# Optimization experiments

Measured on AMD Instinct MI355X. Metric: run time of the kernel, lower is better.

The kernel has to match this reference:

```python
import jax, jax.numpy as jnp
import numpy as np

N, E, G = 50000, 800000, 64
NODE_DIM, EDGE_DIM, HIDDEN, L = 64, 16, 128, 4


def setup_inputs() -> dict:
    key = jax.random.key(0)
    ks = jax.random.split(key, 24)
    s = 0.05
    inp = {
        "x": jax.random.normal(ks[0], (N, NODE_DIM), jnp.float32),
        "pos": jax.random.normal(ks[1], (N, 3), jnp.float32),
        "edge_attr": jax.random.normal(ks[2], (E, EDGE_DIM), jnp.float32),
        "edge_index": jax.random.randint(ks[3], (2, E), 0, N),
        "batch": jnp.sort(jax.random.randint(ks[4], (N,), 0, G)),
        # node encoder
        "enc_W": jax.random.normal(ks[5], (NODE_DIM, HIDDEN), jnp.float32) * s,
        "enc_b": jnp.zeros((HIDDEN,), jnp.float32),
        # per-layer EGNN params, stacked on leading L axis
        "eW1": jax.random.normal(ks[6], (L, 2 * HIDDEN + EDGE_DIM + 1, HIDDEN), jnp.float32) * s,
        "eb1": jnp.zeros((L, HIDDEN), jnp.float32),
        "eW2": jax.random.normal(ks[7], (L, HIDDEN, HIDDEN), jnp.float32) * s,
        "eb2": jnp.zeros((L, HIDDEN), jnp.float32),
        "nW1": jax.random.normal(ks[8], (L, 2 * HIDDEN, HIDDEN), jnp.float32) * s,
        "nb1": jnp.zeros((L, HIDDEN), jnp.float32),
        "nW2": jax.random.normal(ks[9], (L, HIDDEN, HIDDEN), jnp.float32) * s,
        "nb2": jnp.zeros((L, HIDDEN), jnp.float32),
        # readout MLP (hidden*3 -> hidden -> hidden//2 -> 1)
        "rW1": jax.random.normal(ks[10], (3 * HIDDEN, HIDDEN), jnp.float32) * s,
        "rb1": jnp.zeros((HIDDEN,), jnp.float32),
        "rW2": jax.random.normal(ks[11], (HIDDEN, HIDDEN // 2), jnp.float32) * s,
        "rb2": jnp.zeros((HIDDEN // 2,), jnp.float32),
        "rW3": jax.random.normal(ks[12], (HIDDEN // 2, 1), jnp.float32) * s,
        "rb3": jnp.zeros((1,), jnp.float32),
    }
    return inp


def reference(x, pos, edge_attr, enc_W, enc_b, eW1, eb1, eW2, eb2,
              nW1, nb1, nW2, nb2, rW1, rb1, rW2, rb2, rW3, rb3,
              edge_index, batch):
    relu = jax.nn.relu
    src = edge_index[0]  # j (source) in PyG source_to_target flow
    dst = edge_index[1]  # i (target)

    # node encoder (dropout in eval mode = identity)
    h = relu(x @ enc_W + enc_b)

    rel = pos[src] - pos[dst]                       # pos_j - pos_i, [E,3]
    dist2 = jnp.sum(rel * rel, axis=-1, keepdims=True)  # [E,1]

    for l in range(L):
        feat = jnp.concatenate([h[dst], h[src], edge_attr, dist2], axis=-1)
        m = relu(relu(feat @ eW1[l] + eb1[l]) @ eW2[l] + eb2[l])     # [E,H]
        agg = jax.ops.segment_sum(m, dst, num_segments=N)            # [N,H]
        h = relu(jnp.concatenate([h, agg], axis=-1) @ nW1[l] + nb1[l]) @ nW2[l] + nb2[l]

    # global mean / max / add pooling over graphs
    ssum = jax.ops.segment_sum(h, batch, num_segments=G)             # [G,H]
    cnt = jax.ops.segment_sum(jnp.ones((h.shape[0], 1), h.dtype), batch, num_segments=G)
    smean = ssum / jnp.maximum(cnt, 1.0)
    smax = jax.ops.segment_max(h, batch, num_segments=G)
    pooled = jnp.concatenate([smean, smax, ssum], axis=-1)           # [G,3H]

    out = relu(pooled @ rW1 + rb1)
    out = relu(out @ rW2 + rb2)
    return jax.nn.softplus(out @ rW3 + rb3)                          # [G,1]
```

## Files before the change

kernel.cpp:

```cpp
#include <hip/hip_runtime.h>
#include <math.h>

#define NN 50000
#define NE 800000
#define NG 64
#define DIN 64
#define DEA 16
#define H 128
#define NL 4
#define EPB 128
#define MAXD 16

typedef __attribute__((ext_vector_type(8))) short short8;
typedef __attribute__((ext_vector_type(4))) float f32x4;

__device__ __forceinline__ float4 ld4(const float* p) { return *reinterpret_cast<const float4*>(p); }
__device__ __forceinline__ void st4(float* p, float4 v) { *reinterpret_cast<float4*>(p) = v; }
__device__ __forceinline__ void fma4(float4& a, float s, float4 w) {
    a.x = fmaf(s, w.x, a.x); a.y = fmaf(s, w.y, a.y);
    a.z = fmaf(s, w.z, a.z); a.w = fmaf(s, w.w, a.w);
}
__device__ __forceinline__ float4 f4add(float4 a, float4 b) {
    return make_float4(a.x + b.x, a.y + b.y, a.z + b.z, a.w + b.w);
}
__device__ __forceinline__ float4 relu4(float4 a) {
    return make_float4(fmaxf(a.x, 0.f), fmaxf(a.y, 0.f), fmaxf(a.z, 0.f), fmaxf(a.w, 0.f));
}
__device__ __forceinline__ unsigned fkey(float f) {
    unsigned b = __float_as_uint(f);
    return (b & 0x80000000u) ? ~b : (b | 0x80000000u);
}
__device__ __forceinline__ float funkey(unsigned k) {
    unsigned b = (k & 0x80000000u) ? (k ^ 0x80000000u) : ~k;
    return __uint_as_float(b);
}
__device__ __forceinline__ ushort f2bf(float f) {
    unsigned u = __float_as_uint(f);
    return (ushort)((u + 0x7fffu + ((u >> 16) & 1u)) >> 16);
}
__device__ __forceinline__ float bf2f(ushort b) {
    return __uint_as_float(((unsigned)b) << 16);
}

__global__ __launch_bounds__(256) void encoder_kernel(const float* __restrict__ x,
    const float* __restrict__ W, const float* __restrict__ b, float* __restrict__ h)
{
    const int tid = threadIdx.x, q = tid & 31, no = tid >> 5;
    const int nbase = blockIdx.x * 64;
    float4 bv = ld4(b + 4 * q);
    float4 acc[8];
#pragma unroll
    for (int i = 0; i < 8; ++i) acc[i] = bv;
    for (int k4 = 0; k4 < 16; ++k4) {
        const float* wp = W + (4 * k4) * H + 4 * q;
        float4 w0 = ld4(wp), w1 = ld4(wp + H), w2 = ld4(wp + 2 * H), w3 = ld4(wp + 3 * H);
#pragma unroll
        for (int i = 0; i < 8; ++i) {
            int n = nbase + no * 8 + i; n = n < NN ? n : NN - 1;
            float4 a = ld4(x + n * DIN + 4 * k4);
            fma4(acc[i], a.x, w0); fma4(acc[i], a.y, w1);
            fma4(acc[i], a.z, w2); fma4(acc[i], a.w, w3);
        }
    }
#pragma unroll
    for (int i = 0; i < 8; ++i) {
        int n = nbase + no * 8 + i;
        if (n < NN) st4(h + n * H + 4 * q, relu4(acc[i]));
    }
}

__global__ __launch_bounds__(256) void dist2_kernel(const float* __restrict__ pos,
    const int* __restrict__ ei, float* __restrict__ d2)
{
    int e = blockIdx.x * 256 + threadIdx.x;
    if (e >= NE) return;
    int s = ei[e], d = ei[NE + e];
    float dx = pos[s * 3 + 0] - pos[d * 3 + 0];
    float dy = pos[s * 3 + 1] - pos[d * 3 + 1];
    float dz = pos[s * 3 + 2] - pos[d * 3 + 2];
    d2[e] = dx * dx + dy * dy + dz * dz;
}

__global__ __launch_bounds__(256) void hist_kernel(const int* __restrict__ ei, int* __restrict__ deg)
{
    int e = blockIdx.x * 256 + threadIdx.x;
    if (e < NE) atomicAdd(&deg[ei[NE + e]], 1);
}

__global__ __launch_bounds__(1024) void scan_kernel(const int* __restrict__ deg, int* __restrict__ cursor)
{
    __shared__ int tot[1024];
    const int t = threadIdx.x;
    const int CH = (NN + 1023) / 1024;
    const int base = t * CH;
    int s = 0;
    for (int i = 0; i < CH; ++i) {
        int idx = base + i;
        if (idx < NN) s += deg[idx];
    }
    tot[t] = s;
    __syncthreads();
    for (int off = 1; off < 1024; off <<= 1) {
        int v = (t >= off) ? tot[t - off] : 0;
        __syncthreads();
        tot[t] += v;
        __syncthreads();
    }
    int run = (t == 0) ? 0 : tot[t - 1];
    for (int i = 0; i < CH; ++i) {
        int idx = base + i;
        if (idx < NN) { cursor[idx] = run; run += deg[idx]; }
    }
}

__global__ __launch_bounds__(256) void scatter_kernel(const int* __restrict__ ei,
    const float* __restrict__ ea, const float* __restrict__ d2, int* __restrict__ cursor,
    int* __restrict__ src_s, int* __restrict__ dst_s,
    float* __restrict__ ea_s, float* __restrict__ d2_s)
{
    int e = blockIdx.x * 256 + threadIdx.x;
    if (e >= NE) return;
    int s = ei[e], d = ei[NE + e];
    int pos = atomicAdd(&cursor[d], 1);
    src_s[pos] = s; dst_s[pos] = d; d2_s[pos] = d2[e];
    const float4* ev = reinterpret_cast<const float4*>(ea + (size_t)e * DEA);
    float4* ov = reinterpret_cast<float4*>(ea_s + (size_t)pos * DEA);
    ov[0] = ev[0]; ov[1] = ev[1]; ov[2] = ev[2]; ov[3] = ev[3];
}

__global__ __launch_bounds__(256) void wprep_kernel(const float* __restrict__ W,
    ushort* __restrict__ hi, ushort* __restrict__ lo,
    int K, int in_lstride, int out_lstride)
{
    int l = blockIdx.y;
    const float* Wb = W + (size_t)l * in_lstride;
    ushort* hg = hi + (size_t)l * out_lstride;
    ushort* lg = lo + (size_t)l * out_lstride;
    int total = K * 128;
    for (int idx = blockIdx.x * 256 + threadIdx.x; idx < total; idx += gridDim.x * 256) {
        int k = idx >> 7, n = idx & 127;
        float wv = Wb[idx];
        ushort hb = f2bf(wv);
        float rem = wv - bf2f(hb);
        ushort lb = f2bf(rem);
        int panel = k >> 6, kk = k & 63;
        int pos = panel * 8192 + (n << 6) + (kk ^ ((n & 7) << 3));
        hg[pos] = hb; lg[pos] = lb;
    }
}

__global__ __launch_bounds__(512, 4) void proj_mfma_kernel(const float* __restrict__ h,
    const ushort* __restrict__ wdh, const ushort* __restrict__ wdl,
    const ushort* __restrict__ wsh, const ushort* __restrict__ wsl,
    const float* __restrict__ b1,
    ushort* __restrict__ Pdb, ushort* __restrict__ Psb)
{
    __shared__ __align__(16) ushort Afull[128 * 128];
    __shared__ __align__(16) ushort Wh[128 * 64];
    __shared__ __align__(16) ushort Wl[128 * 64];
    const int tid = threadIdx.x;
    const int nbase = blockIdx.x * 128;

    {
        int r = tid >> 2, kq = (tid & 3) * 32;
        int n = nbase + r; n = n < NN ? n : NN - 1;
        const float* src = h + (size_t)n * H + kq;
        int swz = (r & 7) << 3;
#pragma unroll
        for (int j = 0; j < 4; ++j) {
            float4 a = ld4(src + 8 * j);
            float4 b = ld4(src + 8 * j + 4);
            union { ushort u[8]; int4 v; } pk;
            pk.u[0] = f2bf(a.x); pk.u[1] = f2bf(a.y); pk.u[2] = f2bf(a.z); pk.u[3] = f2bf(a.w);
            pk.u[4] = f2bf(b.x); pk.u[5] = f2bf(b.y); pk.u[6] = f2bf(b.z); pk.u[7] = f2bf(b.w);
            *reinterpret_cast<int4*>(&Afull[r * 128 + ((kq + 8 * j) ^ swz)]) = pk.v;
        }
    }

    const int lane = tid & 63, wvx = tid >> 6, colL = lane & 15, g = lane >> 4;
    const int arow = wvx * 16 + colL, aswz = (arow & 7) << 3;
    f32x4 accd[8], accs[8];
#pragma unroll
    for (int nt = 0; nt < 8; ++nt) { accd[nt] = (f32x4){0, 0, 0, 0}; accs[nt] = (f32x4){0, 0, 0, 0}; }

#define PROJ_ROUND(ABUF, HSRC, LSRC, KOFF, ACC)                                         \
    {                                                                                   \
        ((int4*)Wh)[tid] = ((const int4*)(HSRC))[tid];                                  \
        ((int4*)Wh)[tid + 512] = ((const int4*)(HSRC))[tid + 512];                      \
        ((int4*)Wl)[tid] = ((const int4*)(LSRC))[tid];                                  \
        ((int4*)Wl)[tid + 512] = ((const int4*)(LSRC))[tid + 512];                      \
        __syncthreads();                                                                \
        _Pragma("unroll")                                                               \
        for (int ks = 0; ks < 2; ++ks) {                                                \
            int kk0 = ks * 32;                                                          \
            short8 af = *(const short8*)&ABUF[arow * 128 + (((KOFF) + kk0 + 8 * g) ^ aswz)]; \
            _Pragma("unroll")                                                           \
            for (int nt = 0; nt < 8; ++nt) {                                            \
                int brow = nt * 16 + colL;                                              \
                int bidx = brow * 64 + ((kk0 + 8 * g) ^ ((brow & 7) << 3));             \
                short8 bh = *(const short8*)&Wh[bidx];                                  \
                short8 bl = *(const short8*)&Wl[bidx];                                  \
                ACC[nt] = __builtin_amdgcn_mfma_f32_16x16x32_bf16(af, bh, ACC[nt], 0, 0, 0); \
                ACC[nt] = __builtin_amdgcn_mfma_f32_16x16x32_bf16(af, bl, ACC[nt], 0, 0, 0); \
            }                                                                           \
        }                                                                               \
        __syncthreads();                                                                \
    }

    PROJ_ROUND(Afull, wdh, wdl, 0, accd)
    PROJ_ROUND(Afull, wdh + 8192, wdl + 8192, 64, accd)
    PROJ_ROUND(Afull, wsh, wsl, 0, accs)
    PROJ_ROUND(Afull, wsh + 8192, wsl + 8192, 64, accs)

    float b1r[8];
#pragma unroll
    for (int nt = 0; nt < 8; ++nt) b1r[nt] = b1[nt * 16 + colL];

    const int rowb = wvx * 16 + g * 4;
#pragma unroll
    for (int r = 0; r < 4; ++r) {
        int n = nbase + rowb + r;
        if (n < NN) {
#pragma unroll
            for (int nt = 0; nt < 8; ++nt) {
                Pdb[(size_t)n * H + nt * 16 + colL] = f2bf(accd[nt][r] + b1r[nt]);
                Psb[(size_t)n * H + nt * 16 + colL] = f2bf(accs[nt][r]);
            }
        }
    }
}

__global__ __launch_bounds__(512, 4) void edge_mfma_kernel(
    const ushort* __restrict__ Pdb, const ushort* __restrict__ Psb,
    const float* __restrict__ ea_s, const float* __restrict__ d2_s,
    const int* __restrict__ src_s, const int* __restrict__ dst_s,
    const float* __restrict__ W1,
    const ushort* __restrict__ w2hiL, const ushort* __restrict__ w2loL,
    const float* __restrict__ b2, float* __restrict__ agg)
{
    __shared__ __align__(16) ushort tls[EPB * H];
    __shared__ __align__(16) float accb[MAXD * H];

    const int NWG = NE / EPB, QQ = NWG / 8, RR = NWG % 8;
    int orig = blockIdx.x;
    int xcd = orig & 7, ixc = orig >> 3;
    int bswz = (xcd < RR ? xcd * (QQ + 1) : RR * (QQ + 1) + (xcd - RR) * QQ) + ixc;

    const int tid = threadIdx.x, q = tid & 31, eo = tid >> 5;
    const int ebase = bswz * EPB;
    const int lane = tid & 63, wv = tid >> 6;
    const int col = lane & 15, g = lane >> 4;

    st4(&accb[tid * 4], make_float4(0.f, 0.f, 0.f, 0.f));

    const int dfirst = dst_s[ebase];
    const int dlast  = dst_s[ebase + EPB - 1];
    const int dprev  = (ebase > 0) ? dst_s[ebase - 1] : -1;
    const int dnext  = (ebase + EPB < NE) ? dst_s[ebase + EPB] : -1;

    const float* Wea = W1 + 256 * H;
    const float* wdv = W1 + 272 * H;
    float4 wdq = ld4(wdv + 4 * q);

    int srcs[8], dsts8[8];
    float d2v[8];
#pragma unroll
    for (int i = 0; i < 8; ++i) {
        int j = ebase + eo * 8 + i;
        srcs[i] = src_s[j]; dsts8[i] = dst_s[j]; d2v[i] = d2_s[j];
    }
    float4 acc1[8];
#pragma unroll
    for (int i = 0; i < 8; ++i) {
        ushort4 pd4 = *reinterpret_cast<const ushort4*>(&Pdb[(size_t)dsts8[i] * H + 4 * q]);
        ushort4 ps4 = *reinterpret_cast<const ushort4*>(&Psb[(size_t)srcs[i] * H + 4 * q]);
        float4 a;
        a.x = bf2f(pd4.x) + bf2f(ps4.x);
        a.y = bf2f(pd4.y) + bf2f(ps4.y);
        a.z = bf2f(pd4.z) + bf2f(ps4.z);
        a.w = bf2f(pd4.w) + bf2f(ps4.w);
        fma4(a, d2v[i], wdq);
        acc1[i] = a;
    }
#pragma unroll
    for (int k4 = 0; k4 < 4; ++k4) {
        float4 w0 = ld4(Wea + (4 * k4 + 0) * H + 4 * q);
        float4 w1 = ld4(Wea + (4 * k4 + 1) * H + 4 * q);
        float4 w2 = ld4(Wea + (4 * k4 + 2) * H + 4 * q);
        float4 w3 = ld4(Wea + (4 * k4 + 3) * H + 4 * q);
#pragma unroll
        for (int i = 0; i < 8; ++i) {
            int j = ebase + eo * 8 + i;
            float4 av = ld4(ea_s + (size_t)j * DEA + 4 * k4);
            fma4(acc1[i], av.x, w0); fma4(acc1[i], av.y, w1);
            fma4(acc1[i], av.z, w2); fma4(acc1[i], av.w, w3);
        }
    }
#pragma unroll
    for (int i = 0; i < 8; ++i) {
        int el = eo * 8 + i;
        ushort4 tv;
        tv.x = f2bf(fmaxf(acc1[i].x, 0.f)); tv.y = f2bf(fmaxf(acc1[i].y, 0.f));
        tv.z = f2bf(fmaxf(acc1[i].z, 0.f)); tv.w = f2bf(fmaxf(acc1[i].w, 0.f));
        int tidx = el * H + ((4 * q) ^ ((el & 7) << 3));
        *reinterpret_cast<ushort4*>(&tls[tidx]) = tv;
    }

    const int nW = wv * 16 + col;
    const int nswz = (nW & 7) << 3;
    short8 bh[4], bl[4];
#pragma unroll
    for (int ks = 0; ks < 4; ++ks) {
        int kkg = ks * 32 + 8 * g;
        int panel = kkg >> 6, kk = kkg & 63;
        int pos = panel * 8192 + nW * 64 + (kk ^ nswz);
        bh[ks] = *reinterpret_cast<const short8*>(&w2hiL[pos]);
        bl[ks] = *reinterpret_cast<const short8*>(&w2loL[pos]);
    }
    float b2r = b2[nW];

    __syncthreads();

    f32x4 acc[8];
#pragma unroll
    for (int rt = 0; rt < 8; ++rt) acc[rt] = (f32x4){b2r, b2r, b2r, b2r};

    __builtin_amdgcn_s_setprio(1);
#pragma unroll
    for (int rt = 0; rt < 8; ++rt) {
        const int arow = rt * 16 + col;
        const int aswz = (arow & 7) << 3;
#pragma unroll
        for (int ks = 0; ks < 4; ++ks) {
            short8 af = *(const short8*)&tls[arow * H + ((ks * 32 + 8 * g) ^ aswz)];
            acc[rt] = __builtin_amdgcn_mfma_f32_16x16x32_bf16(af, bh[ks], acc[rt], 0, 0, 0);
            acc[rt] = __builtin_amdgcn_mfma_f32_16x16x32_bf16(af, bl[ks], acc[rt], 0, 0, 0);
        }
    }
    __builtin_amdgcn_s_setprio(0);

#pragma unroll
    for (int rt = 0; rt < 8; ++rt) {
        const int ge = ebase + rt * 16 + g * 4;
        int d0 = dst_s[ge + 0], d1 = dst_s[ge + 1];
        int d2i = dst_s[ge + 2], d3 = dst_s[ge + 3];
        float v0 = fmaxf(acc[rt][0], 0.f);
        float v1 = fmaxf(acc[rt][1], 0.f);
        float v2 = fmaxf(acc[rt][2], 0.f);
        float v3 = fmaxf(acc[rt][3], 0.f);
        float vrun = v0;
        int dcur = d0;
#define FLUSH_RUN(DD, VV)                                                          \
        if ((DD) != dcur) {                                                        \
            int sl = dcur - dfirst;                                                \
            if (sl < MAXD) atomicAdd(&accb[sl * H + nW], vrun);                    \
            else atomicAdd(&agg[(size_t)dcur * H + nW], vrun);                     \
            vrun = (VV); dcur = (DD);                                              \
        } else vrun += (VV);
        FLUSH_RUN(d1, v1)
        FLUSH_RUN(d2i, v2)
        FLUSH_RUN(d3, v3)
#undef FLUSH_RUN
        {
            int sl = dcur - dfirst;
            if (sl < MAXD) atomicAdd(&accb[sl * H + nW], vrun);
            else atomicAdd(&agg[(size_t)dcur * H + nW], vrun);
        }
    }

    __syncthreads();

    {
        int span = dlast - dfirst + 1;
        if (span > MAXD) span = MAXD;
        const int colf = tid & 127;
        for (int s = tid >> 7; s < span; s += 4) {
            float v = accb[s * H + colf];
            int d = dfirst + s;
            bool bnd = (s == 0 && dprev == dfirst) || (d == dlast && dnext == dlast);
            if (bnd) atomicAdd(&agg[(size_t)d * H + colf], v);
            else agg[(size_t)d * H + colf] = v;
        }
    }
}

template <int PROJ>
__global__ __launch_bounds__(512, 4) void node_fused_kernel(
    const float* __restrict__ h, const float* __restrict__ agg,
    const ushort* __restrict__ w1h, const ushort* __restrict__ w1l,
    const ushort* __restrict__ w2h, const ushort* __restrict__ w2l,
    const float* __restrict__ b1, const float* __restrict__ b2,
    const ushort* __restrict__ pwdh, const ushort* __restrict__ pwdl,
    const ushort* __restrict__ pwsh, const ushort* __restrict__ pwsl,
    const float* __restrict__ eb1n,
    float* __restrict__ hout, ushort* __restrict__ Pdb, ushort* __restrict__ Psb)
{
    __shared__ __align__(16) ushort Abuf[128 * 64];
    __shared__ __align__(16) ushort ubuf[128 * 128];
    __shared__ __align__(16) ushort Wh[128 * 64];
    __shared__ __align__(16) ushort Wl[128 * 64];
    const int tid = threadIdx.x;
    const int nbase = blockIdx.x * 128;
    const int lane = tid & 63, wvx = tid >> 6, colL = lane & 15, g = lane >> 4;
    const int arow = wvx * 16 + colL, aswz = (arow & 7) << 3;

    f32x4 acc[8];
#pragma unroll
    for (int nt = 0; nt < 8; ++nt) {
        float bb = b1[nt * 16 + colL];
        acc[nt] = (f32x4){bb, bb, bb, bb};
    }

    const int sr = tid >> 2, skq = (tid & 3) * 16;
    const int sswz = (sr & 7) << 3;
    int sn = nbase + sr; sn = sn < NN ? sn : NN - 1;

#pragma unroll
    for (int kp = 0; kp < 4; ++kp) {
        const float* srcb = (kp < 2 ? h : agg);
        const float* src = srcb + (size_t)sn * H + (kp & 1) * 64 + skq;
#pragma unroll
        for (int j = 0; j < 2; ++j) {
            float4 a = ld4(src + 8 * j);
            float4 b = ld4(src + 8 * j + 4);
            union { ushort u[8]; int4 v; } pk;
            pk.u[0] = f2bf(a.x); pk.u[1] = f2bf(a.y); pk.u[2] = f2bf(a.z); pk.u[3] = f2bf(a.w);
            pk.u[4] = f2bf(b.x); pk.u[5] = f2bf(b.y); pk.u[6] = f2bf(b.z); pk.u[7] = f2bf(b.w);
            *reinterpret_cast<int4*>(&Abuf[sr * 64 + ((skq + 8 * j) ^ sswz)]) = pk.v;
        }
        ((int4*)Wh)[tid] = ((const int4*)(w1h + kp * 8192))[tid];
        ((int4*)Wh)[tid + 512] = ((const int4*)(w1h + kp * 8192))[tid + 512];
        ((int4*)Wl)[tid] = ((const int4*)(w1l + kp * 8192))[tid];
        ((int4*)Wl)[tid + 512] = ((const int4*)(w1l + kp * 8192))[tid + 512];
        __syncthreads();
#pragma unroll
        for (int ks = 0; ks < 2; ++ks) {
            int kk0 = ks * 32;
            short8 af = *(const short8*)&Abuf[arow * 64 + ((kk0 + 8 * g) ^ aswz)];
#pragma unroll
            for (int nt = 0; nt < 8; ++nt) {
                int brow = nt * 16 + colL;
                int bidx = brow * 64 + ((kk0 + 8 * g) ^ ((brow & 7) << 3));
                short8 bh = *(const short8*)&Wh[bidx];
                short8 bl = *(const short8*)&Wl[bidx];
                acc[nt] = __builtin_amdgcn_mfma_f32_16x16x32_bf16(af, bh, acc[nt], 0, 0, 0);
                acc[nt] = __builtin_amdgcn_mfma_f32_16x16x32_bf16(af, bl, acc[nt], 0, 0, 0);
            }
        }
        __syncthreads();
    }

    const int rowb = wvx * 16 + g * 4;
#pragma unroll
    for (int r = 0; r < 4; ++r) {
        int row = rowb + r;
        int rs = (row & 7) << 3;
#pragma unroll
        for (int nt = 0; nt < 8; ++nt) {
            ubuf[row * 128 + ((nt * 16 + colL) ^ rs)] = f2bf(fmaxf(acc[nt][r], 0.f));
        }
    }
    __syncthreads();

    f32x4 acc2[8];
#pragma unroll
    for (int nt = 0; nt < 8; ++nt) {
        float bb = b2[nt * 16 + colL];
        acc2[nt] = (f32x4){bb, bb, bb, bb};
    }
#pragma unroll
    for (int kp2 = 0; kp2 < 2; ++kp2) {
        ((int4*)Wh)[tid] = ((const int4*)(w2h + kp2 * 8192))[tid];
        ((int4*)Wh)[tid + 512] = ((const int4*)(w2h + kp2 * 8192))[tid + 512];
        ((int4*)Wl)[tid] = ((const int4*)(w2l + kp2 * 8192))[tid];
        ((int4*)Wl)[tid + 512] = ((const int4*)(w2l + kp2 * 8192))[tid + 512];
        __syncthreads();
#pragma unroll
        for (int ks = 0; ks < 2; ++ks) {
            int kk0 = ks * 32;
            short8 af = *(const short8*)&ubuf[arow * 128 + ((kp2 * 64 + kk0 + 8 * g) ^ aswz)];
#pragma unroll
            for (int nt = 0; nt < 8; ++nt) {
                int brow = nt * 16 + colL;
                int bidx = brow * 64 + ((kk0 + 8 * g) ^ ((brow & 7) << 3));
                short8 bh = *(const short8*)&Wh[bidx];
                short8 bl = *(const short8*)&Wl[bidx];
                acc2[nt] = __builtin_amdgcn_mfma_f32_16x16x32_bf16(af, bh, acc2[nt], 0, 0, 0);
                acc2[nt] = __builtin_amdgcn_mfma_f32_16x16x32_bf16(af, bl, acc2[nt], 0, 0, 0);
            }
        }
        __syncthreads();
    }

#pragma unroll
    for (int r = 0; r < 4; ++r) {
        int n = nbase + rowb + r;
        if (n < NN) {
#pragma unroll
            for (int nt = 0; nt < 8; ++nt)
                hout[(size_t)n * H + nt * 16 + colL] = acc2[nt][r];
        }
    }

    if (PROJ) {
#pragma unroll
        for (int r = 0; r < 4; ++r) {
            int row = rowb + r;
            int rs = (row & 7) << 3;
#pragma unroll
            for (int nt = 0; nt < 8; ++nt) {
                ubuf[row * 128 + ((nt * 16 + colL) ^ rs)] = f2bf(acc2[nt][r]);
            }
        }
        __syncthreads();

        f32x4 accd[8], accs[8];
#pragma unroll
        for (int nt = 0; nt < 8; ++nt) { accd[nt] = (f32x4){0, 0, 0, 0}; accs[nt] = (f32x4){0, 0, 0, 0}; }

        PROJ_ROUND(ubuf, pwdh, pwdl, 0, accd)
        PROJ_ROUND(ubuf, pwdh + 8192, pwdl + 8192, 64, accd)
        PROJ_ROUND(ubuf, pwsh, pwsl, 0, accs)
        PROJ_ROUND(ubuf, pwsh + 8192, pwsl + 8192, 64, accs)

        float b1r[8];
#pragma unroll
        for (int nt = 0; nt < 8; ++nt) b1r[nt] = eb1n[nt * 16 + colL];
#pragma unroll
        for (int r = 0; r < 4; ++r) {
            int n = nbase + rowb + r;
            if (n < NN) {
#pragma unroll
                for (int nt = 0; nt < 8; ++nt) {
                    Pdb[(size_t)n * H + nt * 16 + colL] = f2bf(accd[nt][r] + b1r[nt]);
                    Psb[(size_t)n * H + nt * 16 + colL] = f2bf(accs[nt][r]);
                }
            }
        }
    }
}

__global__ __launch_bounds__(256) void pool_kernel(const float* __restrict__ h,
    const int* __restrict__ batch, float* __restrict__ ssum,
    unsigned int* __restrict__ smaxk, float* __restrict__ cnt)
{
    const int tid = threadIdx.x, j = tid & 127, half = tid >> 7;
    const int nbase = blockIdx.x * 64;
    int cur = -1, rc = 0;
    float s = 0.f, mx = 0.f;
    for (int i = 0; i < 32; ++i) {
        int n = nbase + 2 * i + half;
        if (n >= NN) break;
        int g = batch[n];
        float v = h[(size_t)n * H + j];
        if (g != cur) {
            if (cur >= 0) {
                atomicAdd(&ssum[cur * H + j], s);
                atomicMax(&smaxk[cur * H + j], fkey(mx));
                if (j == 0) atomicAdd(&cnt[cur], (float)rc);
            }
            cur = g; s = v; mx = v; rc = 1;
        } else { s += v; mx = fmaxf(mx, v); rc++; }
    }
    if (cur >= 0) {
        atomicAdd(&ssum[cur * H + j], s);
        atomicMax(&smaxk[cur * H + j], fkey(mx));
        if (j == 0) atomicAdd(&cnt[cur], (float)rc);
    }
}

__global__ __launch_bounds__(128) void readout_kernel(const float* __restrict__ ssum,
    const unsigned int* __restrict__ smaxk, const float* __restrict__ cnt,
    const float* __restrict__ rW1, const float* __restrict__ rb1,
    const float* __restrict__ rW2, const float* __restrict__ rb2,
    const float* __restrict__ rW3, const float* __restrict__ rb3,
    float* __restrict__ out)
{
    __shared__ float p[384], h1[128], h2[64];
    const int g = blockIdx.x, j = threadIdx.x;
    float c = fmaxf(cnt[g], 1.0f);
    float sv = ssum[g * H + j];
    p[j] = sv / c;
    p[128 + j] = funkey(smaxk[g * H + j]);
    p[256 + j] = sv;
    __syncthreads();
    float a = rb1[j];
    for (int k = 0; k < 384; ++k) a = fmaf(p[k], rW1[k * H + j], a);
    h1[j] = fmaxf(a, 0.f);
    __syncthreads();
    if (j < 64) {
        float a2 = rb2[j];
        for (int k = 0; k < 128; ++k) a2 = fmaf(h1[k], rW2[k * 64 + j], a2);
        h2[j] = fmaxf(a2, 0.f);
    }
    __syncthreads();
    if (j < 64) {
        float t = h2[j] * rW3[j];
        for (int off = 32; off; off >>= 1) t += __shfl_down(t, off);
        if (j == 0) {
            float z = t + rb3[0];
            out[g] = z > 20.f ? z : log1pf(expf(z));
        }
    }
}

extern "C" void kernel_launch(void* const* d_in, const int* in_sizes, int n_in,
                              void* d_out, int out_size, void* d_ws, size_t ws_size,
                              hipStream_t stream)
{
    const float* x    = (const float*)d_in[0];
    const float* pos  = (const float*)d_in[1];
    const float* ea   = (const float*)d_in[2];
    const int*   ei   = (const int*)d_in[3];
    const int*   batch= (const int*)d_in[4];
    const float* encW = (const float*)d_in[5];
    const float* encb = (const float*)d_in[6];
    const float* eW1  = (const float*)d_in[7];
    const float* eb1  = (const float*)d_in[8];
    const float* eW2  = (const float*)d_in[9];
    const float* eb2  = (const float*)d_in[10];
    const float* nW1  = (const float*)d_in[11];
    const float* nb1  = (const float*)d_in[12];
    const float* nW2  = (const float*)d_in[13];
    const float* nb2  = (const float*)d_in[14];
    const float* rW1  = (const float*)d_in[15];
    const float* rb1  = (const float*)d_in[16];
    const float* rW2  = (const float*)d_in[17];
    const float* rb2  = (const float*)d_in[18];
    const float* rW3  = (const float*)d_in[19];
    const float* rb3  = (const float*)d_in[20];

    char* w = (char*)d_ws;
    size_t o = 0;
    auto alloc = [&](size_t bytes) -> char* {
        char* p = w + o; o += (bytes + 255) / 256 * 256; return p;
    };
    float* hA   = (float*)alloc((size_t)NN * H * 4);
    float* hB   = (float*)alloc((size_t)NN * H * 4);
    ushort* Pdb = (ushort*)alloc((size_t)NN * H * 2);
    ushort* Psb = (ushort*)alloc((size_t)NN * H * 2);
    float* agg  = (float*)alloc((size_t)NN * H * 4);
    float* d2   = (float*)alloc((size_t)NE * 4);
    float* ssum = (float*)alloc((size_t)NG * H * 4);
    unsigned int* smaxk = (unsigned int*)alloc((size_t)NG * H * 4);
    float* cnt  = (float*)alloc((size_t)NG * 4);
    int*   deg    = (int*)alloc((size_t)NN * 4);
    int*   cursor = (int*)alloc((size_t)NN * 4);
    int*   src_s  = (int*)alloc((size_t)NE * 4);
    int*   dst_s  = (int*)alloc((size_t)NE * 4);
    float* ea_s   = (float*)alloc((size_t)NE * DEA * 4);
    float* d2_s   = (float*)alloc((size_t)NE * 4);
    ushort* w2hi  = (ushort*)alloc((size_t)NL * H * H * 2);
    ushort* w2lo  = (ushort*)alloc((size_t)NL * H * H * 2);
    ushort* nw1hi = (ushort*)alloc((size_t)NL * 256 * H * 2);
    ushort* nw1lo = (ushort*)alloc((size_t)NL * 256 * H * 2);
    ushort* nw2hi = (ushort*)alloc((size_t)NL * H * H * 2);
    ushort* nw2lo = (ushort*)alloc((size_t)NL * H * H * 2);
    ushort* w1dhi = (ushort*)alloc((size_t)NL * H * H * 2);
    ushort* w1dlo = (ushort*)alloc((size_t)NL * H * H * 2);
    ushort* w1shi = (ushort*)alloc((size_t)NL * H * H * 2);
    ushort* w1slo = (ushort*)alloc((size_t)NL * H * H * 2);
    (void)ws_size; (void)in_sizes; (void)n_in; (void)out_size;

    const int NB = (NN + 63) / 64;
    const int NBM = (NN + 127) / 128;
    const int EB = (NE + 255) / 256;

    hipMemsetAsync(deg, 0, (size_t)NN * 4, stream);
    dist2_kernel<<<EB, 256, 0, stream>>>(pos, ei, d2);
    hist_kernel<<<EB, 256, 0, stream>>>(ei, deg);
    scan_kernel<<<1, 1024, 0, stream>>>(deg, cursor);
    scatter_kernel<<<EB, 256, 0, stream>>>(ei, ea, d2, cursor, src_s, dst_s, ea_s, d2_s);

    wprep_kernel<<<dim3(64, NL), 256, 0, stream>>>(eW2, w2hi, w2lo, H, H * H, H * H);
    wprep_kernel<<<dim3(128, NL), 256, 0, stream>>>(nW1, nw1hi, nw1lo, 256, 256 * H, 256 * H);
    wprep_kernel<<<dim3(64, NL), 256, 0, stream>>>(nW2, nw2hi, nw2lo, H, H * H, H * H);
    wprep_kernel<<<dim3(64, NL), 256, 0, stream>>>(eW1, w1dhi, w1dlo, H, 273 * H, H * H);
    wprep_kernel<<<dim3(64, NL), 256, 0, stream>>>(eW1 + 128 * H, w1shi, w1slo, H, 273 * H, H * H);

    encoder_kernel<<<NB, 256, 0, stream>>>(x, encW, encb, hA);

    proj_mfma_kernel<<<NBM, 512, 0, stream>>>(hA,
        w1dhi, w1dlo, w1shi, w1slo, eb1, Pdb, Psb);

    float* hcur = hA;
    float* hnext = hB;
    for (int l = 0; l < NL; ++l) {
        hipMemsetAsync(agg, 0, (size_t)NN * H * 4, stream);
        edge_mfma_kernel<<<NE / EPB, 512, 0, stream>>>(Pdb, Psb, ea_s, d2_s, src_s, dst_s,
            eW1 + (size_t)l * 273 * H, w2hi + (size_t)l * H * H, w2lo + (size_t)l * H * H,
            eb2 + l * H, agg);
        if (l < NL - 1) {
            int ln = l + 1;
            node_fused_kernel<1><<<NBM, 512, 0, stream>>>(hcur, agg,
                nw1hi + (size_t)l * 256 * H, nw1lo + (size_t)l * 256 * H,
                nw2hi + (size_t)l * H * H, nw2lo + (size_t)l * H * H,
                nb1 + l * H, nb2 + l * H,
                w1dhi + (size_t)ln * H * H, w1dlo + (size_t)ln * H * H,
                w1shi + (size_t)ln * H * H, w1slo + (size_t)ln * H * H,
                eb1 + ln * H, hnext, Pdb, Psb);
        } else {
            node_fused_kernel<0><<<NBM, 512, 0, stream>>>(hcur, agg,
                nw1hi + (size_t)l * 256 * H, nw1lo + (size_t)l * 256 * H,
                nw2hi + (size_t)l * H * H, nw2lo + (size_t)l * H * H,
                nb1 + l * H, nb2 + l * H,
                (const ushort*)nullptr, (const ushort*)nullptr,
                (const ushort*)nullptr, (const ushort*)nullptr,
                (const float*)nullptr, hnext, Pdb, Psb);
        }
        float* tmp = hcur; hcur = hnext; hnext = tmp;
    }

    hipMemsetAsync(ssum, 0, (size_t)NG * H * 4, stream);
    hipMemsetAsync(smaxk, 0, (size_t)NG * H * 4, stream);
    hipMemsetAsync(cnt, 0, (size_t)NG * 4, stream);
    pool_kernel<<<NB, 256, 0, stream>>>(hcur, batch, ssum, smaxk, cnt);
    readout_kernel<<<NG, 128, 0, stream>>>(ssum, smaxk, cnt,
        rW1, rb1, rW2, rb2, rW3, rb3, (float*)d_out);
}
```

Baseline: 1.366 ms.

## Compute edge-attr and distance terms of first edge layer with bf16 MFMA

```diff
diff --git a/kernel.cpp b/kernel.cpp
--- a/kernel.cpp
+++ b/kernel.cpp
@@ -9,7 +9,7 @@
 #define H 128
 #define NL 4
 #define EPB 128
-#define MAXD 16
+#define MAXD 12
 
 typedef __attribute__((ext_vector_type(8))) short short8;
 typedef __attribute__((ext_vector_type(4))) float f32x4;
@@ -251,62 +251,48 @@
     const int lane = tid & 63, wv = tid >> 6;
     const int col = lane & 15, g = lane >> 4;
 
-    st4(&accb[tid * 4], make_float4(0.f, 0.f, 0.f, 0.f));
+    if (tid < (MAXD * H) / 4) st4(&accb[tid * 4], make_float4(0.f, 0.f, 0.f, 0.f));
 
     const int dfirst = dst_s[ebase];
     const int dlast  = dst_s[ebase + EPB - 1];
     const int dprev  = (ebase > 0) ? dst_s[ebase - 1] : -1;
     const int dnext  = (ebase + EPB < NE) ? dst_s[ebase + EPB] : -1;
 
+    {
+        int el = tid >> 2, kq = (tid & 3) * 8;
+        union { ushort u[8]; int4 v; } pk;
+        if (kq < 16) {
+            const float* er = ea_s + (size_t)(ebase + el) * DEA + kq;
+            float4 a = ld4(er), b = ld4(er + 4);
+            pk.u[0] = f2bf(a.x); pk.u[1] = f2bf(a.y); pk.u[2] = f2bf(a.z); pk.u[3] = f2bf(a.w);
+            pk.u[4] = f2bf(b.x); pk.u[5] = f2bf(b.y); pk.u[6] = f2bf(b.z); pk.u[7] = f2bf(b.w);
+        } else if (kq == 16) {
+            pk.u[0] = f2bf(d2_s[ebase + el]);
+#pragma unroll
+            for (int j = 1; j < 8; ++j) pk.u[j] = 0;
+        } else {
+#pragma unroll
+            for (int j = 0; j < 8; ++j) pk.u[j] = 0;
+        }
+        int sw = ((el >> 1) & 3) << 3;
+        *reinterpret_cast<int4*>(&tls[el * 32 + (kq ^ sw)]) = pk.v;
+    }
+
+    const int nW = wv * 16 + col;
     const float* Wea = W1 + 256 * H;
     const float* wdv = W1 + 272 * H;
-    float4 wdq = ld4(wdv + 4 * q);
-
-    int srcs[8], dsts8[8];
-    float d2v[8];
-#pragma unroll
-    for (int i = 0; i < 8; ++i) {
-        int j = ebase + eo * 8 + i;
-        srcs[i] = src_s[j]; dsts8[i] = dst_s[j]; d2v[i] = d2_s[j];
-    }
-    float4 acc1[8];
-#pragma unroll
-    for (int i = 0; i < 8; ++i) {
-        ushort4 pd4 = *reinterpret_cast<const ushort4*>(&Pdb[(size_t)dsts8[i] * H + 4 * q]);
-        ushort4 ps4 = *reinterpret_cast<const ushort4*>(&Psb[(size_t)srcs[i] * H + 4 * q]);
-        float4 a;
-        a.x = bf2f(pd4.x) + bf2f(ps4.x);
-        a.y = bf2f(pd4.y) + bf2f(ps4.y);
-        a.z = bf2f(pd4.z) + bf2f(ps4.z);
-        a.w = bf2f(pd4.w) + bf2f(ps4.w);
-        fma4(a, d2v[i], wdq);
-        acc1[i] = a;
-    }
-#pragma unroll
-    for (int k4 = 0; k4 < 4; ++k4) {
-        float4 w0 = ld4(Wea + (4 * k4 + 0) * H + 4 * q);
-        float4 w1 = ld4(Wea + (4 * k4 + 1) * H + 4 * q);
-        float4 w2 = ld4(Wea + (4 * k4 + 2) * H + 4 * q);
-        float4 w3 = ld4(Wea + (4 * k4 + 3) * H + 4 * q);
-#pragma unroll
-        for (int i = 0; i < 8; ++i) {
-            int j = ebase + eo * 8 + i;
-            float4 av = ld4(ea_s + (size_t)j * DEA + 4 * k4);
-            fma4(acc1[i], av.x, w0); fma4(acc1[i], av.y, w1);
-            fma4(acc1[i], av.z, w2); fma4(acc1[i], av.w, w3);
-        }
-    }
-#pragma unroll
-    for (int i = 0; i < 8; ++i) {
-        int el = eo * 8 + i;
-        ushort4 tv;
-        tv.x = f2bf(fmaxf(acc1[i].x, 0.f)); tv.y = f2bf(fmaxf(acc1[i].y, 0.f));
-        tv.z = f2bf(fmaxf(acc1[i].z, 0.f)); tv.w = f2bf(fmaxf(acc1[i].w, 0.f));
-        int tidx = el * H + ((4 * q) ^ ((el & 7) << 3));
-        *reinterpret_cast<ushort4*>(&tls[tidx]) = tv;
-    }
-
-    const int nW = wv * 16 + col;
+    short8 baug;
+    {
+        union { ushort u[8]; short8 s; } bb;
+#pragma unroll
+        for (int j = 0; j < 8; ++j) {
+            int k = 8 * g + j;
+            float v = (k < 16) ? Wea[k * H + nW] : (k == 16 ? wdv[nW] : 0.f);
+            bb.u[j] = f2bf(v);
+        }
+        baug = bb.s;
+    }
+
     const int nswz = (nW & 7) << 3;
     short8 bh[4], bl[4];
 #pragma unroll
@@ -321,6 +307,51 @@
 
     __syncthreads();
 
+    f32x4 tp[8];
+#pragma unroll
+    for (int rt = 0; rt < 8; ++rt) {
+        int ar = rt * 16 + col;
+        int sw = ((ar >> 1) & 3) << 3;
+        short8 aef = *reinterpret_cast<const short8*>(&tls[ar * 32 + ((8 * g) ^ sw)]);
+        tp[rt] = __builtin_amdgcn_mfma_f32_16x16x32_bf16(aef, baug, (f32x4){0.f, 0.f, 0.f, 0.f}, 0, 0, 0);
+    }
+
+    __syncthreads();
+
+#pragma unroll
+    for (int rt = 0; rt < 8; ++rt) {
+#pragma unroll
+        for (int r = 0; r < 4; ++r) {
+            int row = rt * 16 + g * 4 + r;
+            tls[row * H + (nW ^ ((row & 7) << 3))] = f2bf(tp[rt][r]);
+        }
+    }
+
+    __syncthreads();
+
+    int srcs[8], dsts8[8];
+#pragma unroll
+    for (int i = 0; i < 8; ++i) {
+        int j = ebase + eo * 8 + i;
+        srcs[i] = src_s[j]; dsts8[i] = dst_s[j];
+    }
+#pragma unroll
+    for (int i = 0; i < 8; ++i) {
+        int el = eo * 8 + i;
+        int tidx = el * H + ((4 * q) ^ ((el & 7) << 3));
+        ushort4 tpv = *reinterpret_cast<const ushort4*>(&tls[tidx]);
+        ushort4 pd4 = *reinterpret_cast<const ushort4*>(&Pdb[(size_t)dsts8[i] * H + 4 * q]);
+        ushort4 ps4 = *reinterpret_cast<const ushort4*>(&Psb[(size_t)srcs[i] * H + 4 * q]);
+        ushort4 tv;
+        tv.x = f2bf(fmaxf(bf2f(tpv.x) + bf2f(pd4.x) + bf2f(ps4.x), 0.f));
+        tv.y = f2bf(fmaxf(bf2f(tpv.y) + bf2f(pd4.y) + bf2f(ps4.y), 0.f));
+        tv.z = f2bf(fmaxf(bf2f(tpv.z) + bf2f(pd4.z) + bf2f(ps4.z), 0.f));
+        tv.w = f2bf(fmaxf(bf2f(tpv.w) + bf2f(pd4.w) + bf2f(ps4.w), 0.f));
+        *reinterpret_cast<ushort4*>(&tls[tidx]) = tv;
+    }
+
+    __syncthreads();
+
     f32x4 acc[8];
 #pragma unroll
     for (int rt = 0; rt < 8; ++rt) acc[rt] = (f32x4){b2r, b2r, b2r, b2r};
@@ -332,7 +363,7 @@
         const int aswz = (arow & 7) << 3;
 #pragma unroll
         for (int ks = 0; ks < 4; ++ks) {
-            short8 af = *(const short8*)&tls[arow * H + ((ks * 32 + 8 * g) ^ aswz)];
+            short8 af = *reinterpret_cast<const short8*>(&tls[arow * H + ((ks * 32 + 8 * g) ^ aswz)]);
             acc[rt] = __builtin_amdgcn_mfma_f32_16x16x32_bf16(af, bh[ks], acc[rt], 0, 0, 0);
             acc[rt] = __builtin_amdgcn_mfma_f32_16x16x32_bf16(af, bl[ks], acc[rt], 0, 0, 0);
         }
```

Measured after the change: 1.478 ms. +8.2%, slower.
